# Optimization experiments

Hardware: AMD Instinct MI355X
Metric: run time of the kernel (lower is better)

## Reference

```python
import jax, jax.numpy as jnp
import numpy as np
from jax import lax

EPS = 1e-5
DN = ('NCDHW', 'OIDHW', 'NCDHW')


def _instance_norm(x, w, b):
    # normalize over spatial dims per (batch, channel); biased variance like torch
    mu = jnp.mean(x, axis=(2, 3, 4), keepdims=True)
    var = jnp.mean((x - mu) ** 2, axis=(2, 3, 4), keepdims=True)
    xn = (x - mu) * lax.rsqrt(var + EPS)
    return xn * w[None, :, None, None, None] + b[None, :, None, None, None]


def _conv1x1(x, w, b):
    # w: [Cout, Cin]
    y = jnp.einsum('bcdhw,oc->bodhw', x, w)
    return y + b[None, :, None, None, None]


def _dwconv3(x, w, b):
    # depthwise 3x3x3, padding 1; w: [C, 1, 3, 3, 3]
    y = lax.conv_general_dilated(x, w, (1, 1, 1), 'SAME',
                                 dimension_numbers=DN,
                                 feature_group_count=w.shape[0])
    return y + b[None, :, None, None, None]


def setup_inputs() -> dict:
    key = jax.random.key(0)
    ks = jax.random.split(key, 8)
    C, half = 64, 32
    B, D, H, W = 1, 96, 96, 96
    s1 = 1.0 / np.sqrt(C)          # fan_in of 1x1 conv
    s3 = 1.0 / np.sqrt(27.0)       # fan_in of depthwise 3x3x3
    return {
        'x': jax.random.normal(ks[0], (B, C, D, H, W), jnp.float32),
        'norm_w': jnp.ones((C,), jnp.float32),
        'norm_b': jnp.zeros((C,), jnp.float32),
        'in_proj_w': jax.random.normal(ks[1], (C, C), jnp.float32) * s1,
        'in_proj_b': jnp.zeros((C,), jnp.float32),
        'conv_ssm_w': jax.random.normal(ks[2], (half, 1, 3, 3, 3), jnp.float32) * s3,
        'conv_ssm_b': jnp.zeros((half,), jnp.float32),
        'mamba_w': jax.random.normal(ks[3], (half, 1, 3, 3, 3), jnp.float32) * s3,
        'mamba_b': jnp.zeros((half,), jnp.float32),
        'conv_sym_w': jax.random.normal(ks[4], (half, 1, 3, 3, 3), jnp.float32) * s3,
        'conv_sym_b': jnp.zeros((half,), jnp.float32),
        'out_proj_w': jax.random.normal(ks[5], (C, C), jnp.float32) * s1,
        'out_proj_b': jnp.zeros((C,), jnp.float32),
    }


def reference(x, norm_w, norm_b, in_proj_w, in_proj_b,
              conv_ssm_w, conv_ssm_b, mamba_w, mamba_b,
              conv_sym_w, conv_sym_b, out_proj_w, out_proj_b):
    residual = x
    xp = _conv1x1(_instance_norm(x, norm_w, norm_b), in_proj_w, in_proj_b)
    half = xp.shape[1] // 2
    x1, x2 = xp[:, :half], xp[:, half:]
    # SSM branch (TriDirectionalMamba fallback = depthwise conv3)
    x1 = _dwconv3(jax.nn.silu(_dwconv3(x1, conv_ssm_w, conv_ssm_b)), mamba_w, mamba_b)
    # symmetric conv branch
    x2 = jax.nn.silu(_dwconv3(x2, conv_sym_w, conv_sym_b))
    y = _conv1x1(jnp.concatenate([x1, x2], axis=1), out_proj_w, out_proj_b)
    return y + residual
```

## Files before the change

kernel.cpp:

```cpp
#include <hip/hip_runtime.h>

typedef unsigned short u16;
typedef unsigned int u32;
typedef short bf16x8 __attribute__((ext_vector_type(8)));
typedef float f32x16 __attribute__((ext_vector_type(16)));
typedef u16 u16x8 __attribute__((ext_vector_type(8)));

#define DIM 96
#define PLANE (DIM*DIM)
#define S 884736
#define C 64
#define HALF 32
#define PARTS 16
#define EPS 1e-5f
#define DSPLIT 8
#define DCHUNK (DIM/DSPLIT)

#define MFMA32(a,b,c) __builtin_amdgcn_mfma_f32_32x32x16_bf16(a,b,c,0,0,0)

__device__ __forceinline__ u16 f2bf(float f) {
  u32 u = __builtin_bit_cast(u32, f);
  return (u16)((u + 0x7FFFu + ((u >> 16) & 1u)) >> 16);
}
__device__ __forceinline__ float bf2f(u16 h) {
  return __builtin_bit_cast(float, (u32)h << 16);
}
__device__ __forceinline__ u32 cvt_pk_bf16(float lo, float hi) {
  u32 r;
  asm("v_cvt_pk_bf16_f32 %0, %1, %2" : "=v"(r) : "v"(lo), "v"(hi));
  return r;
}
__device__ __forceinline__ float silu(float v) { return v / (1.f + __expf(-v)); }
__device__ __forceinline__ u16x8 zero8() {
  u16x8 z;
  #pragma unroll
  for (int i = 0; i < 8; ++i) z[i] = 0;
  return z;
}
__device__ __forceinline__ void zrow(float* __restrict__ r) {
  #pragma unroll
  for (int i = 0; i < 10; ++i) r[i] = 0.f;
}

__global__ __launch_bounds__(256) void k1_stats(const float* __restrict__ x,
                                                u16* __restrict__ xb,
                                                float* __restrict__ psum,
                                                float* __restrict__ psq) {
  const int bid = blockIdx.x;
  const int ch = bid / PARTS, part = bid % PARTS;
  const int chunk = S / PARTS;
  const size_t base = (size_t)ch * S + (size_t)part * chunk;
  const float4* p = (const float4*)(x + base);
  ushort4* xb4 = (ushort4*)(xb + base);
  const int n4 = chunk / 4;
  float s = 0.f, q = 0.f;
  for (int i = threadIdx.x; i < n4; i += 256) {
    float4 v = p[i];
    s += (v.x + v.y) + (v.z + v.w);
    q += (v.x * v.x + v.y * v.y) + (v.z * v.z + v.w * v.w);
    union { u32 u[2]; ushort4 v4; } o;
    o.u[0] = cvt_pk_bf16(v.x, v.y);
    o.u[1] = cvt_pk_bf16(v.z, v.w);
    xb4[i] = o.v4;
  }
  #pragma unroll
  for (int off = 32; off > 0; off >>= 1) {
    s += __shfl_down(s, off);
    q += __shfl_down(q, off);
  }
  __shared__ float ls[4], lq[4];
  const int wid = threadIdx.x >> 6, lane = threadIdx.x & 63;
  if (lane == 0) { ls[wid] = s; lq[wid] = q; }
  __syncthreads();
  if (threadIdx.x == 0) {
    psum[bid] = (ls[0] + ls[1]) + (ls[2] + ls[3]);
    psq[bid]  = (lq[0] + lq[1]) + (lq[2] + lq[3]);
  }
}

__global__ __launch_bounds__(64) void k1b_prep(const float* __restrict__ psum,
    const float* __restrict__ psq,
    const float* __restrict__ norm_w, const float* __restrict__ norm_b,
    const float* __restrict__ in_w, const float* __restrict__ in_b,
    const float* __restrict__ out_w,
    u16* __restrict__ Wp, float* __restrict__ biasp, u16* __restrict__ Wo) {
  __shared__ float a_s[C], b2_s[C];
  const int t = threadIdx.x;
  float s = 0.f, q = 0.f;
  for (int i = 0; i < PARTS; ++i) { s += psum[t * PARTS + i]; q += psq[t * PARTS + i]; }
  const float inv = 1.f / (float)S;
  const float mu = s * inv;
  const float var = q * inv - mu * mu;
  const float rsig = rsqrtf(var + EPS);
  const float a = norm_w[t] * rsig;
  const float b2 = norm_b[t] - mu * a;
  a_s[t] = a; b2_s[t] = b2;
  __syncthreads();
  float bp = in_b[t];
  for (int c = 0; c < C; ++c) {
    const float w = in_w[t * C + c];
    Wp[t * C + c] = f2bf(w * a_s[c]);
    bp += b2_s[c] * w;
    Wo[t * C + c] = f2bf(out_w[t * C + c]);
  }
  biasp[t] = bp;
}

__global__ __launch_bounds__(256) void k2_mfma(const u16* __restrict__ xb,
    const u16* __restrict__ Wp, const float* __restrict__ biasp,
    u16* __restrict__ xp) {
  const int lane = threadIdx.x & 63, wid = threadIdx.x >> 6;
  const int n = lane & 31, hf = lane >> 5;
  const int v0 = blockIdx.x * 256 + wid * 64;
  bf16x8 A[2][4];
  #pragma unroll
  for (int t = 0; t < 2; ++t)
    #pragma unroll
    for (int s = 0; s < 4; ++s)
      A[t][s] = *(const bf16x8*)(Wp + (t * 32 + n) * C + s * 16 + hf * 8);

  f32x16 accE[2], accO[2];
  #pragma unroll
  for (int t = 0; t < 2; ++t)
    #pragma unroll
    for (int r = 0; r < 16; ++r) {
      const float b = biasp[t * 32 + (r & 3) + 8 * (r >> 2) + 4 * hf];
      accE[t][r] = b; accO[t][r] = b;
    }

  #pragma unroll
  for (int s = 0; s < 4; ++s) {
    union { u16 u[8]; bf16x8 v; } BE, BO;
    #pragma unroll
    for (int j = 0; j < 8; ++j) {
      const u32 xv = *(const u32*)(xb + (size_t)(s * 16 + hf * 8 + j) * S + v0 + 2 * n);
      BE.u[j] = (u16)(xv & 0xFFFFu); BO.u[j] = (u16)(xv >> 16);
    }
    #pragma unroll
    for (int t = 0; t < 2; ++t) {
      accE[t] = MFMA32(A[t][s], BE.v, accE[t]);
      accO[t] = MFMA32(A[t][s], BO.v, accO[t]);
    }
  }
  #pragma unroll
  for (int t = 0; t < 2; ++t)
    #pragma unroll
    for (int r = 0; r < 16; ++r) {
      const int o = t * 32 + (r & 3) + 8 * (r >> 2) + 4 * hf;
      *(u32*)(xp + (size_t)o * S + v0 + 2 * n) = cvt_pk_bf16(accE[t][r], accO[t][r]);
    }
}

__device__ __forceinline__ void fma_row8(float* __restrict__ a,
    const float* __restrict__ r, float t0, float t1, float t2) {
  #pragma unroll
  for (int i = 0; i < 8; ++i) a[i] += t0 * r[i] + t1 * r[i + 1] + t2 * r[i + 2];
}

template<bool SILU>
__global__ __launch_bounds__(192) void dwconv(const u16* __restrict__ srcA,
    const float* __restrict__ kwA, const float* __restrict__ bA,
    u16* __restrict__ dstA,
    const float* __restrict__ kwB, const float* __restrict__ bB,
    u16* __restrict__ dstB) {
  const int c = blockIdx.z;
  const u16* src = srcA + (size_t)c * S;
  u16* dst; const float* kwp; float bias;
  if (c < HALF) { dst = dstA + (size_t)c * S;          kwp = kwA + c * 27;          bias = bA[c]; }
  else          { dst = dstB + (size_t)(c - HALF) * S; kwp = kwB + (c - HALF) * 27; bias = bB[c - HALF]; }
  float kw[27];
  #pragma unroll
  for (int i = 0; i < 27; ++i) kw[i] = kwp[i];

  const int w8 = threadIdx.x * 8;
  const int h  = blockIdx.x * 16 + threadIdx.y;
  const bool hm = h > 0, hp = h < DIM - 1;
  const bool wlo = w8 > 0, whi = w8 < DIM - 8;
  const int d0 = blockIdx.y * DCHUNK;

  float Wn[3][3][10];
  u16x8 Rm[3]; u16 Rlo[3], Rhi[3];

  #define RAWLOAD(PPTR) { \
    const u16* _p = (PPTR); \
    if (hm) { Rm[0] = *(const u16x8*)(_p - DIM); Rlo[0] = wlo ? _p[-DIM - 1] : (u16)0; Rhi[0] = whi ? _p[-DIM + 8] : (u16)0; } \
    else    { Rm[0] = zero8(); Rlo[0] = 0; Rhi[0] = 0; } \
    {         Rm[1] = *(const u16x8*)(_p);       Rlo[1] = wlo ? _p[-1]       : (u16)0; Rhi[1] = whi ? _p[8]        : (u16)0; } \
    if (hp) { Rm[2] = *(const u16x8*)(_p + DIM); Rlo[2] = wlo ? _p[DIM - 1]  : (u16)0; Rhi[2] = whi ? _p[DIM + 8]  : (u16)0; } \
    else    { Rm[2] = zero8(); Rlo[2] = 0; Rhi[2] = 0; } }

  #define CONVERT(PP) { \
    _Pragma("unroll") \
    for (int k = 0; k < 3; ++k) { \
      Wn[PP][k][0] = bf2f(Rlo[k]); \
      _Pragma("unroll") \
      for (int i = 0; i < 8; ++i) Wn[PP][k][1 + i] = bf2f(Rm[k][i]); \
      Wn[PP][k][9] = bf2f(Rhi[k]); } }

  const u16* pb0 = src + h * DIM + w8;
  u16* db = dst + (size_t)d0 * PLANE + h * DIM + w8;

  if (d0 > 0) { RAWLOAD(pb0 + (size_t)(d0 - 1) * PLANE); CONVERT(2); }
  else        { zrow(Wn[2][0]); zrow(Wn[2][1]); zrow(Wn[2][2]); }
  RAWLOAD(pb0 + (size_t)d0 * PLANE); CONVERT(0);
  const u16* pb = pb0 + (size_t)(d0 + 1) * PLANE;
  RAWLOAD(pb);

  #define STEP(D, PM, PC, PP) { \
    if ((D) + 1 < DIM) { CONVERT(PP); } \
    else { zrow(Wn[PP][0]); zrow(Wn[PP][1]); zrow(Wn[PP][2]); } \
    pb += PLANE; \
    if ((D) + 2 < DIM) RAWLOAD(pb); \
    float a[8]; \
    _Pragma("unroll") \
    for (int i = 0; i < 8; ++i) a[i] = bias; \
    fma_row8(a, Wn[PM][0], kw[0],  kw[1],  kw[2]); \
    fma_row8(a, Wn[PM][1], kw[3],  kw[4],  kw[5]); \
    fma_row8(a, Wn[PM][2], kw[6],  kw[7],  kw[8]); \
    fma_row8(a, Wn[PC][0], kw[9],  kw[10], kw[11]); \
    fma_row8(a, Wn[PC][1], kw[12], kw[13], kw[14]); \
    fma_row8(a, Wn[PC][2], kw[15], kw[16], kw[17]); \
    fma_row8(a, Wn[PP][0], kw[18], kw[19], kw[20]); \
    fma_row8(a, Wn[PP][1], kw[21], kw[22], kw[23]); \
    fma_row8(a, Wn[PP][2], kw[24], kw[25], kw[26]); \
    if (SILU) { \
      _Pragma("unroll") \
      for (int i = 0; i < 8; ++i) a[i] = silu(a[i]); \
    } \
    union { u32 u[4]; u16x8 v; } o; \
    _Pragma("unroll") \
    for (int i = 0; i < 4; ++i) o.u[i] = cvt_pk_bf16(a[2 * i], a[2 * i + 1]); \
    *(u16x8*)db = o.v; \
    db += PLANE; }

  #pragma unroll 1
  for (int it3 = 0; it3 < DCHUNK; it3 += 3) {
    const int d = d0 + it3;
    STEP(d,     2, 0, 1);
    STEP(d + 1, 0, 1, 2);
    STEP(d + 2, 1, 2, 0);
  }
  #undef STEP
  #undef CONVERT
  #undef RAWLOAD
}

__global__ __launch_bounds__(256) void k4b_mfma(const u16* __restrict__ z_lo,
    const u16* __restrict__ z_hi, const u16* __restrict__ xb,
    const u16* __restrict__ Wo, const float* __restrict__ ob,
    float* __restrict__ out) {
  const int lane = threadIdx.x & 63, wid = threadIdx.x >> 6;
  const int n = lane & 31, hf = lane >> 5;
  const int v0 = blockIdx.x * 256 + wid * 64;
  bf16x8 A[2][4];
  #pragma unroll
  for (int t = 0; t < 2; ++t)
    #pragma unroll
    for (int s = 0; s < 4; ++s)
      A[t][s] = *(const bf16x8*)(Wo + (t * 32 + n) * C + s * 16 + hf * 8);

  f32x16 accE[2], accO[2];
  #pragma unroll
  for (int t = 0; t < 2; ++t)
    #pragma unroll
    for (int r = 0; r < 16; ++r) {
      const float b = ob[t * 32 + (r & 3) + 8 * (r >> 2) + 4 * hf];
      accE[t][r] = b; accO[t][r] = b;
    }

  #pragma unroll
  for (int s = 0; s < 4; ++s) {
    const u16* zbase = (s < 2) ? z_lo + (size_t)(s * 16) * S
                               : z_hi + (size_t)((s - 2) * 16) * S;
    union { u16 u[8]; bf16x8 v; } BE, BO;
    #pragma unroll
    for (int j = 0; j < 8; ++j) {
      const u32 zv = *(const u32*)(zbase + (size_t)(hf * 8 + j) * S + v0 + 2 * n);
      BE.u[j] = (u16)(zv & 0xFFFFu); BO.u[j] = (u16)(zv >> 16);
    }
    #pragma unroll
    for (int t = 0; t < 2; ++t) {
      accE[t] = MFMA32(A[t][s], BE.v, accE[t]);
      accO[t] = MFMA32(A[t][s], BO.v, accO[t]);
    }
  }
  #pragma unroll
  for (int t = 0; t < 2; ++t)
    #pragma unroll
    for (int r = 0; r < 16; ++r) {
      const int o = t * 32 + (r & 3) + 8 * (r >> 2) + 4 * hf;
      const u32 xr = *(const u32*)(xb + (size_t)o * S + v0 + 2 * n);
      float2 ov;
      ov.x = accE[t][r] + bf2f((u16)(xr & 0xFFFFu));
      ov.y = accO[t][r] + bf2f((u16)(xr >> 16));
      *(float2*)(out + (size_t)o * S + v0 + 2 * n) = ov;
    }
}

extern "C" void kernel_launch(void* const* d_in, const int* in_sizes, int n_in,
                              void* d_out, int out_size, void* d_ws, size_t ws_size,
                              hipStream_t stream) {
  const float* x      = (const float*)d_in[0];
  const float* norm_w = (const float*)d_in[1];
  const float* norm_b = (const float*)d_in[2];
  const float* in_w   = (const float*)d_in[3];
  const float* in_b   = (const float*)d_in[4];
  const float* ssm_w  = (const float*)d_in[5];
  const float* ssm_b  = (const float*)d_in[6];
  const float* mam_w  = (const float*)d_in[7];
  const float* mam_b  = (const float*)d_in[8];
  const float* sym_w  = (const float*)d_in[9];
  const float* sym_b  = (const float*)d_in[10];
  const float* out_w  = (const float*)d_in[11];
  const float* out_b  = (const float*)d_in[12];
  float* out = (float*)d_out;

  u16* xb   = (u16*)d_ws;
  u16* xp   = xb + (size_t)C * S;
  u16* t1   = xp + (size_t)C * S;
  u16* z_hi = t1 + (size_t)HALF * S;
  u16* z_lo = xp;
  float* psum  = (float*)(z_hi + (size_t)HALF * S);
  float* psq   = psum + C * PARTS;
  u16* Wp      = (u16*)(psq + C * PARTS);
  u16* Wo      = Wp + C * C;
  float* biasp = (float*)(Wo + C * C);

  k1_stats<<<C * PARTS, 256, 0, stream>>>(x, xb, psum, psq);
  k1b_prep<<<1, 64, 0, stream>>>(psum, psq, norm_w, norm_b, in_w, in_b, out_w,
                                 Wp, biasp, Wo);
  k2_mfma<<<S / 256, 256, 0, stream>>>(xb, Wp, biasp, xp);
  dwconv<true><<<dim3(DIM / 16, DSPLIT, C), dim3(12, 16, 1), 0, stream>>>(
      xp, ssm_w, ssm_b, t1, sym_w, sym_b, z_hi);
  dwconv<false><<<dim3(DIM / 16, DSPLIT, HALF), dim3(12, 16, 1), 0, stream>>>(
      t1, mam_w, mam_b, z_lo, mam_w, mam_b, z_lo);
  k4b_mfma<<<S / 256, 256, 0, stream>>>(z_lo, z_hi, xb, Wo, out_b, out);
}
```

Measured before the change: 395.1 us.

## Restructure depthwise conv to scatter each plane into rolling partial accumulators

The depthwise 3x3x3 conv no longer keeps three converted input planes in registers. Each newly loaded plane is applied once to three rolling 8-wide partial sums (output planes d-1, d, d+1), which removes the 3x30-float window. The launch bounds now request 2 blocks per SM and the depth split is halved, so each block handles more planes and reloads fewer halo planes. The FMA count is unchanged, but register pressure drops, and the coarser depth split cuts the number of blocks in the grid.

```diff
diff --git a/kernel.cpp b/kernel.cpp
--- a/kernel.cpp
+++ b/kernel.cpp
@@ -13,7 +13,7 @@
 #define HALF 32
 #define PARTS 16
 #define EPS 1e-5f
-#define DSPLIT 8
+#define DSPLIT 4
 #define DCHUNK (DIM/DSPLIT)
 
 #define MFMA32(a,b,c) __builtin_amdgcn_mfma_f32_32x32x16_bf16(a,b,c,0,0,0)
@@ -36,10 +36,6 @@
   #pragma unroll
   for (int i = 0; i < 8; ++i) z[i] = 0;
   return z;
-}
-__device__ __forceinline__ void zrow(float* __restrict__ r) {
-  #pragma unroll
-  for (int i = 0; i < 10; ++i) r[i] = 0.f;
 }
 
 __global__ __launch_bounds__(256) void k1_stats(const float* __restrict__ x,
@@ -158,7 +154,7 @@
 }
 
 template<bool SILU>
-__global__ __launch_bounds__(192) void dwconv(const u16* __restrict__ srcA,
+__global__ __launch_bounds__(192, 2) void dwconv(const u16* __restrict__ srcA,
     const float* __restrict__ kwA, const float* __restrict__ bA,
     u16* __restrict__ dstA,
     const float* __restrict__ kwB, const float* __restrict__ bB,
@@ -178,8 +174,9 @@
   const bool wlo = w8 > 0, whi = w8 < DIM - 8;
   const int d0 = blockIdx.y * DCHUNK;
 
-  float Wn[3][3][10];
   u16x8 Rm[3]; u16 Rlo[3], Rhi[3];
+  float r0[10], r1[10], r2[10];
+  float A[8], B[8], o8[8];
 
   #define RAWLOAD(PPTR) { \
     const u16* _p = (PPTR); \
@@ -189,58 +186,67 @@
     if (hp) { Rm[2] = *(const u16x8*)(_p + DIM); Rlo[2] = wlo ? _p[DIM - 1]  : (u16)0; Rhi[2] = whi ? _p[DIM + 8]  : (u16)0; } \
     else    { Rm[2] = zero8(); Rlo[2] = 0; Rhi[2] = 0; } }
 
-  #define CONVERT(PP) { \
+  #define CONVERT() { \
+    r0[0] = bf2f(Rlo[0]); r1[0] = bf2f(Rlo[1]); r2[0] = bf2f(Rlo[2]); \
     _Pragma("unroll") \
-    for (int k = 0; k < 3; ++k) { \
-      Wn[PP][k][0] = bf2f(Rlo[k]); \
-      _Pragma("unroll") \
-      for (int i = 0; i < 8; ++i) Wn[PP][k][1 + i] = bf2f(Rm[k][i]); \
-      Wn[PP][k][9] = bf2f(Rhi[k]); } }
+    for (int i = 0; i < 8; ++i) { \
+      r0[1 + i] = bf2f(Rm[0][i]); r1[1 + i] = bf2f(Rm[1][i]); r2[1 + i] = bf2f(Rm[2][i]); } \
+    r0[9] = bf2f(Rhi[0]); r1[9] = bf2f(Rhi[1]); r2[9] = bf2f(Rhi[2]); }
+
+  #define CBLK(ACC, K0) \
+    fma_row8(ACC, r0, kw[(K0) + 0], kw[(K0) + 1], kw[(K0) + 2]); \
+    fma_row8(ACC, r1, kw[(K0) + 3], kw[(K0) + 4], kw[(K0) + 5]); \
+    fma_row8(ACC, r2, kw[(K0) + 6], kw[(K0) + 7], kw[(K0) + 8]);
 
   const u16* pb0 = src + h * DIM + w8;
-  u16* db = dst + (size_t)d0 * PLANE + h * DIM + w8;
-
-  if (d0 > 0) { RAWLOAD(pb0 + (size_t)(d0 - 1) * PLANE); CONVERT(2); }
-  else        { zrow(Wn[2][0]); zrow(Wn[2][1]); zrow(Wn[2][2]); }
-  RAWLOAD(pb0 + (size_t)d0 * PLANE); CONVERT(0);
+
+  if (d0 > 0) {
+    RAWLOAD(pb0 + (size_t)(d0 - 1) * PLANE); CONVERT();
+    #pragma unroll
+    for (int i = 0; i < 8; ++i) B[i] = bias;
+    CBLK(B, 0);
+  } else {
+    #pragma unroll
+    for (int i = 0; i < 8; ++i) B[i] = bias;
+  }
+  RAWLOAD(pb0 + (size_t)d0 * PLANE); CONVERT();
+  #pragma unroll
+  for (int i = 0; i < 8; ++i) { A[i] = B[i]; B[i] = bias; }
+  CBLK(A, 9);
+  CBLK(B, 0);
   const u16* pb = pb0 + (size_t)(d0 + 1) * PLANE;
   RAWLOAD(pb);
-
-  #define STEP(D, PM, PC, PP) { \
-    if ((D) + 1 < DIM) { CONVERT(PP); } \
-    else { zrow(Wn[PP][0]); zrow(Wn[PP][1]); zrow(Wn[PP][2]); } \
-    pb += PLANE; \
-    if ((D) + 2 < DIM) RAWLOAD(pb); \
-    float a[8]; \
-    _Pragma("unroll") \
-    for (int i = 0; i < 8; ++i) a[i] = bias; \
-    fma_row8(a, Wn[PM][0], kw[0],  kw[1],  kw[2]); \
-    fma_row8(a, Wn[PM][1], kw[3],  kw[4],  kw[5]); \
-    fma_row8(a, Wn[PM][2], kw[6],  kw[7],  kw[8]); \
-    fma_row8(a, Wn[PC][0], kw[9],  kw[10], kw[11]); \
-    fma_row8(a, Wn[PC][1], kw[12], kw[13], kw[14]); \
-    fma_row8(a, Wn[PC][2], kw[15], kw[16], kw[17]); \
-    fma_row8(a, Wn[PP][0], kw[18], kw[19], kw[20]); \
-    fma_row8(a, Wn[PP][1], kw[21], kw[22], kw[23]); \
-    fma_row8(a, Wn[PP][2], kw[24], kw[25], kw[26]); \
-    if (SILU) { \
-      _Pragma("unroll") \
-      for (int i = 0; i < 8; ++i) a[i] = silu(a[i]); \
-    } \
-    union { u32 u[4]; u16x8 v; } o; \
-    _Pragma("unroll") \
-    for (int i = 0; i < 4; ++i) o.u[i] = cvt_pk_bf16(a[2 * i], a[2 * i + 1]); \
-    *(u16x8*)db = o.v; \
-    db += PLANE; }
+  u16* db = dst + (size_t)d0 * PLANE + h * DIM + w8;
 
   #pragma unroll 1
-  for (int it3 = 0; it3 < DCHUNK; it3 += 3) {
-    const int d = d0 + it3;
-    STEP(d,     2, 0, 1);
-    STEP(d + 1, 0, 1, 2);
-    STEP(d + 2, 1, 2, 0);
-  }
-  #undef STEP
+  for (int d = d0; d < d0 + DCHUNK; ++d) {
+    if (d + 1 < DIM) { CONVERT(); }
+    else {
+      #pragma unroll
+      for (int i = 0; i < 10; ++i) { r0[i] = 0.f; r1[i] = 0.f; r2[i] = 0.f; }
+    }
+    pb += PLANE;
+    if (d + 2 < DIM) RAWLOAD(pb);
+    #pragma unroll
+    for (int i = 0; i < 8; ++i) o8[i] = A[i];
+    CBLK(o8, 18);
+    #pragma unroll
+    for (int i = 0; i < 8; ++i) A[i] = B[i];
+    CBLK(A, 9);
+    #pragma unroll
+    for (int i = 0; i < 8; ++i) B[i] = bias;
+    CBLK(B, 0);
+    if (SILU) {
+      #pragma unroll
+      for (int i = 0; i < 8; ++i) o8[i] = silu(o8[i]);
+    }
+    union { u32 u[4]; u16x8 v; } o;
+    #pragma unroll
+    for (int i = 0; i < 4; ++i) o.u[i] = cvt_pk_bf16(o8[2 * i], o8[2 * i + 1]);
+    *(u16x8*)db = o.v;
+    db += PLANE;
+  }
+  #undef CBLK
   #undef CONVERT
   #undef RAWLOAD
 }
```

Result: no change. 402.3 us (+1.8%).
